# Kernel tuning notes

Measured on AMD Instinct MI355X. Metric: run time of the kernel, lower is better.

## Reference

```python
import jax, jax.numpy as jnp
import numpy as np

HIDDEN = 4096
NH = 32          # query heads
NKV = 2          # kv heads (multi_query_group_num)
HD = 128         # head dim
ROT = HD // 2    # GLM style: rotary applied to first half of head_dim
THETA = 10000.0
SCALE = HD ** -0.5
G = NH // NKV    # query heads per kv group


def _glm_rope(x, positions):
    # x: [B, S, N, HD]; GPT-J interleaved rotation on the first ROT dims.
    inv_freq = 1.0 / (THETA ** (jnp.arange(0, ROT, 2, dtype=jnp.float32) / ROT))  # [ROT//2]
    ang = positions.astype(jnp.float32)[..., None] * inv_freq                      # [B, S, ROT//2]
    cos = jnp.cos(ang)[:, :, None, :]
    sin = jnp.sin(ang)[:, :, None, :]
    xr, xp = x[..., :ROT], x[..., ROT:]
    x1, x2 = xr[..., 0::2], xr[..., 1::2]
    r1 = x1 * cos - x2 * sin
    r2 = x1 * sin + x2 * cos
    xr = jnp.stack([r1, r2], axis=-1).reshape(xr.shape)  # re-interleave
    return jnp.concatenate([xr, xp], axis=-1)


def setup_inputs() -> dict:
    key = jax.random.key(0)
    k1, k2, k3, k4 = jax.random.split(key, 4)
    B, S = 2, 2048
    positions = jnp.broadcast_to(jnp.arange(S, dtype=jnp.int64), (B, S))
    hidden_states = jax.random.normal(k1, (B, S, HIDDEN), dtype=jnp.float32)
    qkv_out = NH * HD + 2 * NKV * HD  # 4608
    w_qkv = jax.random.normal(k2, (qkv_out, HIDDEN), dtype=jnp.float32) * 0.02
    b_qkv = jax.random.normal(k3, (qkv_out,), dtype=jnp.float32) * 0.02
    w_dense = jax.random.normal(k4, (HIDDEN, NH * HD), dtype=jnp.float32) * 0.02
    return {"positions": positions, "hidden_states": hidden_states,
            "w_qkv": w_qkv, "b_qkv": b_qkv, "w_dense": w_dense}


def reference(positions, hidden_states, w_qkv, b_qkv, w_dense):
    B, S, _ = hidden_states.shape
    mixed = hidden_states @ w_qkv.T + b_qkv                      # [B,S,4608]
    q = mixed[..., : NH * HD].reshape(B, S, NH, HD)
    k = mixed[..., NH * HD: NH * HD + NKV * HD].reshape(B, S, NKV, HD)
    v = mixed[..., NH * HD + NKV * HD:].reshape(B, S, NKV, HD)

    q = _glm_rope(q, positions)
    k = _glm_rope(k, positions)

    # GQA: view q as [B, S, NKV, G, HD]
    qg = q.reshape(B, S, NKV, G, HD)
    scores = jnp.einsum('bqkgd,bskd->bkgqs', qg, k) * SCALE      # [B,NKV,G,S,S]
    causal = jnp.tril(jnp.ones((S, S), dtype=bool))
    scores = jnp.where(causal, scores, jnp.finfo(scores.dtype).min)
    probs = jax.nn.softmax(scores, axis=-1)
    ctx = jnp.einsum('bkgqs,bskd->bqkgd', probs, v)              # [B,S,NKV,G,HD]
    ctx = ctx.reshape(B, S, NH * HD)
    return ctx @ w_dense.T                                       # [B,S,HIDDEN]
```

## Files before the change

kernel.cpp:

```cpp
#include <hip/hip_runtime.h>

typedef float f32x4 __attribute__((ext_vector_type(4)));
typedef __bf16 bf16x8 __attribute__((ext_vector_type(8)));
typedef unsigned short u16x4 __attribute__((ext_vector_type(4)));
typedef unsigned short u16x8 __attribute__((ext_vector_type(8)));

#define HIDDEN 4096
#define NH 32
#define NKV 2
#define HD 128
#define SLEN 2048
#define BATCH 2
#define QKV_OUT 4608
#define MROWS 4096
#define ATT_SCALE 0.08838834764831845f
#define KCHUNK 1024

__device__ __forceinline__ unsigned short f2bf(float f) {
  unsigned int u = __float_as_uint(f);
  u += 0x7fffu + ((u >> 16) & 1u);
  return (unsigned short)(u >> 16);
}

__device__ __forceinline__ float bf2f(unsigned short s) {
  return __uint_as_float((unsigned int)s << 16);
}

__device__ __forceinline__ void gload16(const void* g, void* l) {
  __builtin_amdgcn_global_load_lds((const __attribute__((address_space(1))) void*)g,
                                   (__attribute__((address_space(3))) void*)l, 16, 0, 0);
}

__global__ __launch_bounds__(256) void cvt3_f32_bf16(
    const float* __restrict__ s0, unsigned short* __restrict__ d0, int n0,
    const float* __restrict__ s1, unsigned short* __restrict__ d1, int n1,
    const float* __restrict__ s2, unsigned short* __restrict__ d2, int n2) {
  const int ntot = n0 + n1 + n2;
  const int stride = gridDim.x * blockDim.x;
  for (int i = blockIdx.x * blockDim.x + threadIdx.x; i < ntot; i += stride) {
    const float* src;
    unsigned short* dst;
    int j = i;
    if (j < n0) { src = s0; dst = d0; }
    else if (j < n0 + n1) { j -= n0; src = s1; dst = d1; }
    else { j -= n0 + n1; src = s2; dst = d2; }
    float4 v = reinterpret_cast<const float4*>(src)[j];
    u16x4 o;
    o[0] = f2bf(v.x); o[1] = f2bf(v.y); o[2] = f2bf(v.z); o[3] = f2bf(v.w);
    reinterpret_cast<u16x4*>(dst)[j] = o;
  }
}

__global__ __launch_bounds__(512) void gemm_bf16_mfma(
    const unsigned short* __restrict__ A, const unsigned short* __restrict__ B,
    const float* __restrict__ bias, void* __restrict__ Cout, int M, int N, int K,
    int c_bf16) {
  __shared__ unsigned short as_[128 * 32];
  __shared__ unsigned short bs_[256 * 32];
  const int tid = threadIdx.x;
  const int wave = tid >> 6;
  const int lane = tid & 63;
  const int lr = lane & 15, lg = lane >> 4;
  const int m0 = blockIdx.y * 128;
  const int n0 = blockIdx.x * 256;
  const int wm = (wave >> 2) * 64;
  const int wn = (wave & 3) * 64;

  f32x4 acc[4][4] = {};

  const int srow = tid >> 2;
  const int scol = (tid & 3) * 8;
  unsigned short* lA = as_ + wave * 512;
  unsigned short* lB0 = bs_ + wave * 512;
  unsigned short* lB1 = bs_ + 128 * 32 + wave * 512;

  const int nk = K >> 5;
  for (int kt = 0; kt < nk; ++kt) {
    const int kb = kt << 5;
    __syncthreads();
    gload16(A + (size_t)(m0 + srow) * K + kb + scol, lA);
    gload16(B + (size_t)(n0 + srow) * K + kb + scol, lB0);
    gload16(B + (size_t)(n0 + 128 + srow) * K + kb + scol, lB1);
    __syncthreads();

    bf16x8 aF[4], bF[4];
#pragma unroll
    for (int m4 = 0; m4 < 4; ++m4)
      aF[m4] = *reinterpret_cast<const bf16x8*>(
          &as_[(wm + m4 * 16 + lr) * 32 + lg * 8]);
#pragma unroll
    for (int n4 = 0; n4 < 4; ++n4)
      bF[n4] = *reinterpret_cast<const bf16x8*>(
          &bs_[(wn + n4 * 16 + lr) * 32 + lg * 8]);
#pragma unroll
    for (int m4 = 0; m4 < 4; ++m4)
#pragma unroll
      for (int n4 = 0; n4 < 4; ++n4)
        acc[m4][n4] =
            __builtin_amdgcn_mfma_f32_16x16x32_bf16(aF[m4], bF[n4], acc[m4][n4], 0, 0, 0);
  }

#pragma unroll
  for (int m4 = 0; m4 < 4; ++m4) {
#pragma unroll
    for (int n4 = 0; n4 < 4; ++n4) {
      const int col = n0 + wn + n4 * 16 + lr;
      const float bv = bias ? bias[col] : 0.0f;
      if (c_bf16) {
        unsigned short* C = (unsigned short*)Cout;
#pragma unroll
        for (int r = 0; r < 4; ++r) {
          const int row = m0 + wm + m4 * 16 + lg * 4 + r;
          C[(size_t)row * N + col] = f2bf(acc[m4][n4][r] + bv);
        }
      } else {
        float* C = (float*)Cout;
#pragma unroll
        for (int r = 0; r < 4; ++r) {
          const int row = m0 + wm + m4 * 16 + lg * 4 + r;
          C[(size_t)row * N + col] = acc[m4][n4][r] + bv;
        }
      }
    }
  }
}

__global__ __launch_bounds__(256) void prep_qkv(const unsigned short* __restrict__ mixed,
                                                const int* __restrict__ positions,
                                                unsigned short* __restrict__ Qb,
                                                unsigned short* __restrict__ Kb,
                                                unsigned short* __restrict__ Vt) {
  const int m = blockIdx.x;
  const int b = m >> 11, s = m & 2047;
  const float pos = (float)positions[m];
  const int dp = threadIdx.x & 63;
  const bool rope_lane = (dp < 32);
  float sn = 0.0f, cs = 1.0f;
  if (rope_lane) {
    const float inv = __expf(-(float)dp * 0.28782313662425572f);
    sincosf(pos * inv, &sn, &cs);
  }
  const unsigned int* row =
      reinterpret_cast<const unsigned int*>(mixed + (size_t)m * QKV_OUT);
#pragma unroll
  for (int it = 0; it < 9; ++it) {
    const int p = it * 256 + threadIdx.x;
    const int col = p * 2;
    const unsigned int pk = row[p];
    float r1 = bf2f((unsigned short)(pk & 0xffffu));
    float r2 = bf2f((unsigned short)(pk >> 16));
    const int d = col & 127;
    const bool is_v = (col >= NH * HD + NKV * HD);
    if (rope_lane && !is_v) {
      const float x1 = r1, x2 = r2;
      r1 = x1 * cs - x2 * sn;
      r2 = x1 * sn + x2 * cs;
    }
    if (col < NH * HD) {
      r1 *= ATT_SCALE;
      r2 *= ATT_SCALE;
      const int h = col >> 7;
      const unsigned int packed = (unsigned int)f2bf(r1) | ((unsigned int)f2bf(r2) << 16);
      *reinterpret_cast<unsigned int*>(
          &Qb[((size_t)(b * NH + h) * SLEN + s) * HD + d]) = packed;
    } else if (!is_v) {
      const int kv = (col - NH * HD) >> 7;
      const unsigned int packed = (unsigned int)f2bf(r1) | ((unsigned int)f2bf(r2) << 16);
      *reinterpret_cast<unsigned int*>(
          &Kb[((size_t)(b * NKV + kv) * SLEN + s) * HD + d]) = packed;
    } else {
      const int kv = (col - NH * HD - NKV * HD) >> 7;
      unsigned short* vb = Vt + ((size_t)(b * NKV + kv) * HD) * SLEN + s;
      vb[(size_t)d * SLEN] = f2bf(r1);
      vb[(size_t)(d + 1) * SLEN] = f2bf(r2);
    }
  }
}

__global__ __launch_bounds__(512) void flash_mfma(const unsigned short* __restrict__ Qb,
                                                  const unsigned short* __restrict__ Kb,
                                                  const unsigned short* __restrict__ Vt,
                                                  unsigned short* __restrict__ ctx,
                                                  unsigned short* __restrict__ Om,
                                                  float* __restrict__ Ml) {
  __shared__ unsigned short Ks[2][64 * 128];
  __shared__ unsigned short Vs[128 * 64];
  __shared__ unsigned short Ps[8][16 * 64];

  const int tid = threadIdx.x;
  const int wave = tid >> 6, lane = tid & 63;
  const int lr = lane & 15, lg = lane >> 4;

  const int i = blockIdx.x;
  int qt, c;
  if (i < 8) { qt = 15 - i; c = 0; }
  else if (i < 16) { qt = 23 - i; c = 1; }
  else { qt = 23 - i; c = 0; }
  const int h = blockIdx.y, b = blockIdx.z;
  const int kv = h >> 4;
  const int q0 = qt * 128;
  const int s_begin = c * KCHUNK;
  const int s_end = min(KCHUNK * (c + 1), q0 + 128);
  const int nkt = (s_end - s_begin) >> 6;
  const bool single = (c == 0) && (s_end == q0 + 128);
  const int qbw = q0 + wave * 16;

  const unsigned short* Kbase = Kb + (size_t)(b * NKV + kv) * SLEN * HD;
  const unsigned short* Vbase = Vt + (size_t)(b * NKV + kv) * HD * SLEN;

  bf16x8 bQ[4];
  {
    const unsigned short* qp =
        Qb + ((size_t)(b * NH + h) * SLEN + qbw + lr) * HD;
#pragma unroll
    for (int ks = 0; ks < 4; ++ks)
      bQ[ks] = *reinterpret_cast<const bf16x8*>(qp + lg * 8 + ks * 32);
  }

  f32x4 accO[8] = {};
  float mi = -1e30f, li = 0.0f;

  const int vrow_off = lane >> 3, vchunk = lane & 7;
#define STAGE_K(cb, t)                                                                  \
  {                                                                                     \
    const int ss = s_begin + (t) * 64;                                                  \
    _Pragma("unroll") for (int si = 0; si < 2; ++si) {                                  \
      const int krow = wave * 8 + si * 4 + lg;                                          \
      gload16(Kbase + (size_t)(ss + krow) * HD + ((lr ^ (krow & 7)) << 3),              \
              &Ks[cb][(wave * 8 + si * 4) * 128]);                                      \
    }                                                                                   \
  }
#define STAGE_V(t)                                                                      \
  {                                                                                     \
    const int ss = s_begin + (t) * 64;                                                  \
    _Pragma("unroll") for (int si = 0; si < 2; ++si) {                                  \
      const int drow = wave * 16 + si * 8 + vrow_off;                                   \
      gload16(Vbase + (size_t)drow * SLEN + ss + ((vchunk ^ (drow & 7)) << 3),          \
              &Vs[(wave * 16 + si * 8) * 64]);                                          \
    }                                                                                   \
  }

  STAGE_K(0, 0);
  __syncthreads();

  unsigned short* Pw = Ps[wave];

  for (int kt = 0; kt < nkt; ++kt) {
    const int cur = kt & 1;
    const int s0 = s_begin + kt * 64;
    STAGE_V(kt);
    if (kt + 1 < nkt) STAGE_K(cur ^ 1, kt + 1);
    const bool part = (s0 < qbw + 16);

    f32x4 accS[4] = {};
    if (part) {
      bf16x8 aK[4][4];
#pragma unroll
      for (int kb = 0; kb < 4; ++kb)
#pragma unroll
        for (int ks = 0; ks < 4; ++ks)
          aK[kb][ks] = *reinterpret_cast<const bf16x8*>(
              &Ks[cur][(kb * 16 + lr) * 128 + (((ks * 4 + lg) ^ (lr & 7)) << 3)]);
#pragma unroll
      for (int kb = 0; kb < 4; ++kb)
#pragma unroll
        for (int ks = 0; ks < 4; ++ks)
          accS[kb] = __builtin_amdgcn_mfma_f32_16x16x32_bf16(aK[kb][ks], bQ[ks], accS[kb], 0, 0, 0);
    }

    __syncthreads();

    if (part) {
      const int qrow = qbw + lr;
      float v[16];
#pragma unroll
      for (int kb = 0; kb < 4; ++kb)
#pragma unroll
        for (int r = 0; r < 4; ++r) v[kb * 4 + r] = accS[kb][r];
      if (s0 + 63 > qbw) {
#pragma unroll
        for (int kb = 0; kb < 4; ++kb)
#pragma unroll
          for (int r = 0; r < 4; ++r)
            if (s0 + kb * 16 + lg * 4 + r > qrow) v[kb * 4 + r] = -1e30f;
      }
      float m16 = v[0];
#pragma unroll
      for (int i2 = 1; i2 < 16; ++i2) m16 = fmaxf(m16, v[i2]);
      m16 = fmaxf(m16, __shfl_xor(m16, 16));
      m16 = fmaxf(m16, __shfl_xor(m16, 32));
      const float mnew = fmaxf(mi, m16);
      const float cf = __expf(mi - mnew);
      mi = mnew;
      float rs = 0.0f;
#pragma unroll
      for (int i2 = 0; i2 < 16; ++i2) {
        const float p = __expf(v[i2] - mnew);
        v[i2] = p;
        rs += p;
      }
      rs += __shfl_xor(rs, 16);
      rs += __shfl_xor(rs, 32);
      li = li * cf + rs;
#pragma unroll
      for (int n8 = 0; n8 < 8; ++n8) accO[n8] *= cf;
#pragma unroll
      for (int kb = 0; kb < 4; ++kb) {
        const int slot = (kb * 2 + (lg >> 1)) ^ (lr & 7);
        u16x4 pk;
        pk[0] = f2bf(v[kb * 4 + 0]); pk[1] = f2bf(v[kb * 4 + 1]);
        pk[2] = f2bf(v[kb * 4 + 2]); pk[3] = f2bf(v[kb * 4 + 3]);
        *reinterpret_cast<u16x4*>(&Pw[lr * 64 + slot * 8 + (lg & 1) * 4]) = pk;
      }

      bf16x8 pa[2];
#pragma unroll
      for (int ks = 0; ks < 2; ++ks)
        pa[ks] = *reinterpret_cast<const bf16x8*>(
            &Pw[lr * 64 + (((ks * 4 + lg) ^ (lr & 7)) << 3)]);
#pragma unroll
      for (int ks = 0; ks < 2; ++ks) {
#pragma unroll
        for (int n8 = 0; n8 < 8; ++n8) {
          bf16x8 aV = *reinterpret_cast<const bf16x8*>(
              &Vs[(n8 * 16 + lr) * 64 + (((ks * 4 + lg) ^ (lr & 7)) << 3)]);
          accO[n8] = __builtin_amdgcn_mfma_f32_16x16x32_bf16(aV, pa[ks], accO[n8], 0, 0, 0);
        }
      }
    }

    __syncthreads();
  }
#undef STAGE_K
#undef STAGE_V

  if (single) {
    const float inv = 1.0f / li;
    unsigned short* orow =
        ctx + (size_t)(b * SLEN + qbw + lr) * HIDDEN + h * HD + lg * 4;
#pragma unroll
    for (int n8 = 0; n8 < 8; ++n8) {
      u16x4 o;
#pragma unroll
      for (int r = 0; r < 4; ++r) o[r] = f2bf(accO[n8][r] * inv);
      *reinterpret_cast<u16x4*>(orow + n8 * 16) = o;
    }
  } else {
    const int row1k = qbw + lr - 1024;
    const size_t pbase = (size_t)((b * NH + h) * 2 + c) * 1024 + row1k;
    if (lg == 0) {
      Ml[pbase * 2] = mi;
      Ml[pbase * 2 + 1] = li;
    }
    unsigned short* prow = Om + pbase * 128 + lg * 4;
#pragma unroll
    for (int n8 = 0; n8 < 8; ++n8) {
      u16x4 o;
#pragma unroll
      for (int r = 0; r < 4; ++r) o[r] = f2bf(accO[n8][r]);
      *reinterpret_cast<u16x4*>(prow + n8 * 16) = o;
    }
  }
}

__global__ __launch_bounds__(256) void combine_partials(
    const unsigned short* __restrict__ Om, const float* __restrict__ Ml,
    unsigned short* __restrict__ ctx) {
  const int g = blockIdx.x * 64 + (threadIdx.x >> 2);
  const int p = threadIdx.x & 3;
  const int row1k = g & 1023;
  const int h = (g >> 10) & 31;
  const int b = g >> 15;
  const size_t base0 = (size_t)((b * NH + h) * 2 + 0) * 1024 + row1k;
  const size_t base1 = (size_t)((b * NH + h) * 2 + 1) * 1024 + row1k;
  const float m0 = Ml[base0 * 2], l0 = Ml[base0 * 2 + 1];
  const float m1 = Ml[base1 * 2], l1 = Ml[base1 * 2 + 1];
  const float mx = fmaxf(m0, m1);
  const float w0 = __expf(m0 - mx), w1 = __expf(m1 - mx);
  const float inv = 1.0f / (w0 * l0 + w1 * l1);
  const unsigned short* n0 = Om + base0 * 128 + p * 32;
  const unsigned short* n1 = Om + base1 * 128 + p * 32;
  unsigned short* orow =
      ctx + (size_t)(b * SLEN + 1024 + row1k) * HIDDEN + h * HD + p * 32;
#pragma unroll
  for (int cch = 0; cch < 4; ++cch) {
    u16x8 a = *reinterpret_cast<const u16x8*>(n0 + cch * 8);
    u16x8 d = *reinterpret_cast<const u16x8*>(n1 + cch * 8);
    u16x8 o;
#pragma unroll
    for (int j = 0; j < 8; ++j)
      o[j] = f2bf((w0 * bf2f(a[j]) + w1 * bf2f(d[j])) * inv);
    *reinterpret_cast<u16x8*>(orow + cch * 8) = o;
  }
}

extern "C" void kernel_launch(void* const* d_in, const int* in_sizes, int n_in,
                              void* d_out, int out_size, void* d_ws, size_t ws_size,
                              hipStream_t stream) {
  const int* positions = (const int*)d_in[0];
  const float* hidden = (const float*)d_in[1];
  const float* w_qkv = (const float*)d_in[2];
  const float* b_qkv = (const float*)d_in[3];
  const float* w_dense = (const float*)d_in[4];
  float* out = (float*)d_out;

  char* ws = (char*)d_ws;
  size_t off = 0;
  unsigned short* mixed = (unsigned short*)(ws + off);
  off += (size_t)MROWS * QKV_OUT * 4;
  unsigned short* h_bf = (unsigned short*)(ws + off);
  off += (size_t)MROWS * HIDDEN * 2;
  unsigned short* wq_bf = (unsigned short*)(ws + off);
  off += (size_t)QKV_OUT * HIDDEN * 2;
  unsigned short* wd_bf = (unsigned short*)(ws + off);
  off += (size_t)HIDDEN * HIDDEN * 2;
  unsigned short* Kb = (unsigned short*)(ws + off);
  off += (size_t)BATCH * NKV * SLEN * HD * 2;
  unsigned short* Vt = (unsigned short*)(ws + off);
  off += (size_t)BATCH * NKV * SLEN * HD * 2;
  unsigned short* Qb = h_bf;
  unsigned short* ctx_bf = mixed;
  unsigned short* Om = wq_bf;
  float* Ml = (float*)((char*)mixed + 36 * 1024 * 1024);

  cvt3_f32_bf16<<<2048, 256, 0, stream>>>(hidden, h_bf, MROWS * HIDDEN / 4,
                                          w_qkv, wq_bf, QKV_OUT * HIDDEN / 4,
                                          w_dense, wd_bf, HIDDEN * HIDDEN / 4);

  gemm_bf16_mfma<<<dim3(QKV_OUT / 256, MROWS / 128), 512, 0, stream>>>(
      h_bf, wq_bf, b_qkv, mixed, MROWS, QKV_OUT, HIDDEN, 1);

  prep_qkv<<<MROWS, 256, 0, stream>>>(mixed, positions, Qb, Kb, Vt);

  flash_mfma<<<dim3(24, NH, BATCH), 512, 0, stream>>>(Qb, Kb, Vt, ctx_bf, Om, Ml);

  combine_partials<<<1024, 256, 0, stream>>>(Om, Ml, ctx_bf);

  gemm_bf16_mfma<<<dim3(HIDDEN / 256, MROWS / 128), 512, 0, stream>>>(
      ctx_bf, wd_bf, nullptr, out, MROWS, HIDDEN, HIDDEN, 0);
}
```

Baseline: 609.2 us.

## Fuse RoPE/QKV scatter into GEMM epilogue and widen GEMM K-tile with swizzle

```diff
diff --git a/kernel.cpp b/kernel.cpp
--- a/kernel.cpp
+++ b/kernel.cpp
@@ -51,12 +51,23 @@
   }
 }
 
+__global__ __launch_bounds__(256) void build_trig(float2* __restrict__ tab) {
+  const int idx = blockIdx.x * 256 + threadIdx.x;
+  const int p = idx >> 5, j = idx & 31;
+  const float inv = __expf(-(float)j * 0.28782313662425572f);
+  float sn, cs;
+  sincosf((float)p * inv, &sn, &cs);
+  tab[idx] = make_float2(cs, sn);
+}
+
 __global__ __launch_bounds__(512) void gemm_bf16_mfma(
     const unsigned short* __restrict__ A, const unsigned short* __restrict__ B,
     const float* __restrict__ bias, void* __restrict__ Cout, int M, int N, int K,
-    int c_bf16) {
-  __shared__ unsigned short as_[128 * 32];
-  __shared__ unsigned short bs_[256 * 32];
+    int mode, const float2* __restrict__ tab, const int* __restrict__ positions,
+    unsigned short* __restrict__ Qb, unsigned short* __restrict__ Kb,
+    unsigned short* __restrict__ Vt) {
+  __shared__ unsigned short as_[128 * 64];
+  __shared__ unsigned short bs_[256 * 64];
   const int tid = threadIdx.x;
   const int wave = tid >> 6;
   const int lane = tid & 63;
@@ -68,53 +79,52 @@
 
   f32x4 acc[4][4] = {};
 
-  const int srow = tid >> 2;
-  const int scol = (tid & 3) * 8;
+  const int srow8 = tid >> 3;
+  const int schunk = (tid & 7) ^ (srow8 & 7);
+  const int scol = schunk * 8;
   unsigned short* lA = as_ + wave * 512;
-  unsigned short* lB0 = bs_ + wave * 512;
-  unsigned short* lB1 = bs_ + 128 * 32 + wave * 512;
-
-  const int nk = K >> 5;
+  unsigned short* lB = bs_ + wave * 512;
+
+  const int nk = K >> 6;
   for (int kt = 0; kt < nk; ++kt) {
-    const int kb = kt << 5;
+    const int kb = kt << 6;
     __syncthreads();
-    gload16(A + (size_t)(m0 + srow) * K + kb + scol, lA);
-    gload16(B + (size_t)(n0 + srow) * K + kb + scol, lB0);
-    gload16(B + (size_t)(n0 + 128 + srow) * K + kb + scol, lB1);
+    gload16(A + (size_t)(m0 + srow8) * K + kb + scol, lA);
+    gload16(A + (size_t)(m0 + 64 + srow8) * K + kb + scol, lA + 4096);
+    gload16(B + (size_t)(n0 + srow8) * K + kb + scol, lB);
+    gload16(B + (size_t)(n0 + 64 + srow8) * K + kb + scol, lB + 4096);
+    gload16(B + (size_t)(n0 + 128 + srow8) * K + kb + scol, lB + 8192);
+    gload16(B + (size_t)(n0 + 192 + srow8) * K + kb + scol, lB + 12288);
     __syncthreads();
 
-    bf16x8 aF[4], bF[4];
-#pragma unroll
-    for (int m4 = 0; m4 < 4; ++m4)
-      aF[m4] = *reinterpret_cast<const bf16x8*>(
-          &as_[(wm + m4 * 16 + lr) * 32 + lg * 8]);
-#pragma unroll
-    for (int n4 = 0; n4 < 4; ++n4)
-      bF[n4] = *reinterpret_cast<const bf16x8*>(
-          &bs_[(wn + n4 * 16 + lr) * 32 + lg * 8]);
-#pragma unroll
-    for (int m4 = 0; m4 < 4; ++m4)
+#pragma unroll
+    for (int kk = 0; kk < 2; ++kk) {
+      bf16x8 aF[4], bF[4];
+#pragma unroll
+      for (int m4 = 0; m4 < 4; ++m4)
+        aF[m4] = *reinterpret_cast<const bf16x8*>(
+            &as_[(wm + m4 * 16 + lr) * 64 + (((kk * 4 + lg) ^ (lr & 7)) << 3)]);
 #pragma unroll
       for (int n4 = 0; n4 < 4; ++n4)
-        acc[m4][n4] =
-            __builtin_amdgcn_mfma_f32_16x16x32_bf16(aF[m4], bF[n4], acc[m4][n4], 0, 0, 0);
-  }
-
-#pragma unroll
-  for (int m4 = 0; m4 < 4; ++m4) {
-#pragma unroll
-    for (int n4 = 0; n4 < 4; ++n4) {
-      const int col = n0 + wn + n4 * 16 + lr;
-      const float bv = bias ? bias[col] : 0.0f;
-      if (c_bf16) {
-        unsigned short* C = (unsigned short*)Cout;
-#pragma unroll
-        for (int r = 0; r < 4; ++r) {
-          const int row = m0 + wm + m4 * 16 + lg * 4 + r;
-          C[(size_t)row * N + col] = f2bf(acc[m4][n4][r] + bv);
-        }
-      } else {
-        float* C = (float*)Cout;
+        bF[n4] = *reinterpret_cast<const bf16x8*>(
+            &bs_[(wn + n4 * 16 + lr) * 64 + (((kk * 4 + lg) ^ (lr & 7)) << 3)]);
+#pragma unroll
+      for (int m4 = 0; m4 < 4; ++m4)
+#pragma unroll
+        for (int n4 = 0; n4 < 4; ++n4)
+          acc[m4][n4] =
+              __builtin_amdgcn_mfma_f32_16x16x32_bf16(aF[m4], bF[n4], acc[m4][n4], 0, 0, 0);
+    }
+  }
+
+  if (mode == 0) {
+    float* C = (float*)Cout;
+#pragma unroll
+    for (int m4 = 0; m4 < 4; ++m4) {
+#pragma unroll
+      for (int n4 = 0; n4 < 4; ++n4) {
+        const int col = n0 + wn + n4 * 16 + lr;
+        const float bv = bias ? bias[col] : 0.0f;
 #pragma unroll
         for (int r = 0; r < 4; ++r) {
           const int row = m0 + wm + m4 * 16 + lg * 4 + r;
@@ -122,57 +132,54 @@
         }
       }
     }
-  }
-}
-
-__global__ __launch_bounds__(256) void prep_qkv(const unsigned short* __restrict__ mixed,
-                                                const int* __restrict__ positions,
-                                                unsigned short* __restrict__ Qb,
-                                                unsigned short* __restrict__ Kb,
-                                                unsigned short* __restrict__ Vt) {
-  const int m = blockIdx.x;
-  const int b = m >> 11, s = m & 2047;
-  const float pos = (float)positions[m];
-  const int dp = threadIdx.x & 63;
-  const bool rope_lane = (dp < 32);
-  float sn = 0.0f, cs = 1.0f;
-  if (rope_lane) {
-    const float inv = __expf(-(float)dp * 0.28782313662425572f);
-    sincosf(pos * inv, &sn, &cs);
-  }
-  const unsigned int* row =
-      reinterpret_cast<const unsigned int*>(mixed + (size_t)m * QKV_OUT);
-#pragma unroll
-  for (int it = 0; it < 9; ++it) {
-    const int p = it * 256 + threadIdx.x;
-    const int col = p * 2;
-    const unsigned int pk = row[p];
-    float r1 = bf2f((unsigned short)(pk & 0xffffu));
-    float r2 = bf2f((unsigned short)(pk >> 16));
-    const int d = col & 127;
-    const bool is_v = (col >= NH * HD + NKV * HD);
-    if (rope_lane && !is_v) {
-      const float x1 = r1, x2 = r2;
-      r1 = x1 * cs - x2 * sn;
-      r2 = x1 * sn + x2 * cs;
-    }
-    if (col < NH * HD) {
-      r1 *= ATT_SCALE;
-      r2 *= ATT_SCALE;
-      const int h = col >> 7;
-      const unsigned int packed = (unsigned int)f2bf(r1) | ((unsigned int)f2bf(r2) << 16);
-      *reinterpret_cast<unsigned int*>(
-          &Qb[((size_t)(b * NH + h) * SLEN + s) * HD + d]) = packed;
-    } else if (!is_v) {
-      const int kv = (col - NH * HD) >> 7;
-      const unsigned int packed = (unsigned int)f2bf(r1) | ((unsigned int)f2bf(r2) << 16);
-      *reinterpret_cast<unsigned int*>(
-          &Kb[((size_t)(b * NKV + kv) * SLEN + s) * HD + d]) = packed;
-    } else {
-      const int kv = (col - NH * HD - NKV * HD) >> 7;
-      unsigned short* vb = Vt + ((size_t)(b * NKV + kv) * HD) * SLEN + s;
-      vb[(size_t)d * SLEN] = f2bf(r1);
-      vb[(size_t)(d + 1) * SLEN] = f2bf(r2);
+  } else {
+#pragma unroll
+    for (int m4 = 0; m4 < 4; ++m4) {
+      const int rowb = m0 + wm + m4 * 16 + lg * 4;
+      const int bb = rowb >> 11;
+      const int ss = rowb & 2047;
+      int pos[4];
+#pragma unroll
+      for (int r = 0; r < 4; ++r) pos[r] = positions[rowb + r];
+#pragma unroll
+      for (int n4 = 0; n4 < 4; ++n4) {
+        const int col = n0 + wn + n4 * 16 + lr;
+        const float bv = bias[col];
+        float val[4];
+#pragma unroll
+        for (int r = 0; r < 4; ++r) val[r] = acc[m4][n4][r] + bv;
+        const int d = col & 127;
+        const bool isv = (col >= NH * HD + NKV * HD);
+        const bool isq = (col < NH * HD);
+        if (d < 64 && !isv) {
+          const int j = d >> 1;
+#pragma unroll
+          for (int r = 0; r < 4; ++r) {
+            const float2 t = tab[pos[r] * 32 + j];
+            const float other = __shfl_xor(val[r], 1);
+            val[r] = (col & 1) ? (other * t.y + val[r] * t.x)
+                               : (val[r] * t.x - other * t.y);
+          }
+        }
+        if (isq) {
+          const int hh = col >> 7;
+          unsigned short* q = Qb + ((size_t)(bb * NH + hh) * SLEN + ss) * HD + d;
+#pragma unroll
+          for (int r = 0; r < 4; ++r) q[(size_t)r * HD] = f2bf(val[r] * ATT_SCALE);
+        } else if (!isv) {
+          const int kvh = (col - NH * HD) >> 7;
+          unsigned short* k = Kb + ((size_t)(bb * NKV + kvh) * SLEN + ss) * HD + d;
+#pragma unroll
+          for (int r = 0; r < 4; ++r) k[(size_t)r * HD] = f2bf(val[r]);
+        } else {
+          const int kvh = (col - NH * HD - NKV * HD) >> 7;
+          u16x4 o;
+#pragma unroll
+          for (int r = 0; r < 4; ++r) o[r] = f2bf(val[r]);
+          *reinterpret_cast<u16x4*>(
+              &Vt[((size_t)(bb * NKV + kvh) * HD + d) * SLEN + ss]) = o;
+        }
+      }
     }
   }
 }
@@ -210,8 +217,7 @@
 
   bf16x8 bQ[4];
   {
-    const unsigned short* qp =
-        Qb + ((size_t)(b * NH + h) * SLEN + qbw + lr) * HD;
+    const unsigned short* qp = Qb + ((size_t)(b * NH + h) * SLEN + qbw + lr) * HD;
 #pragma unroll
     for (int ks = 0; ks < 4; ++ks)
       bQ[ks] = *reinterpret_cast<const bf16x8*>(qp + lg * 8 + ks * 32);
@@ -418,24 +424,29 @@
   off += (size_t)BATCH * NKV * SLEN * HD * 2;
   unsigned short* Vt = (unsigned short*)(ws + off);
   off += (size_t)BATCH * NKV * SLEN * HD * 2;
+  float2* trig = (float2*)(ws + off);
+  off += (size_t)2048 * 32 * 8;
   unsigned short* Qb = h_bf;
-  unsigned short* ctx_bf = mixed;
+  Qb = mixed;
+  unsigned short* ctx_bf = mixed + (size_t)MROWS * HIDDEN;
   unsigned short* Om = wq_bf;
-  float* Ml = (float*)((char*)mixed + 36 * 1024 * 1024);
+  float* Ml = (float*)(ws + off);
+  off += (size_t)BATCH * NH * 2 * 1024 * 2 * 4;
 
   cvt3_f32_bf16<<<2048, 256, 0, stream>>>(hidden, h_bf, MROWS * HIDDEN / 4,
                                           w_qkv, wq_bf, QKV_OUT * HIDDEN / 4,
                                           w_dense, wd_bf, HIDDEN * HIDDEN / 4);
+  build_trig<<<256, 256, 0, stream>>>(trig);
 
   gemm_bf16_mfma<<<dim3(QKV_OUT / 256, MROWS / 128), 512, 0, stream>>>(
-      h_bf, wq_bf, b_qkv, mixed, MROWS, QKV_OUT, HIDDEN, 1);
-
-  prep_qkv<<<MROWS, 256, 0, stream>>>(mixed, positions, Qb, Kb, Vt);
+      h_bf, wq_bf, b_qkv, nullptr, MROWS, QKV_OUT, HIDDEN, 2, trig, positions,
+      Qb, Kb, Vt);
 
   flash_mfma<<<dim3(24, NH, BATCH), 512, 0, stream>>>(Qb, Kb, Vt, ctx_bf, Om, Ml);
 
   combine_partials<<<1024, 256, 0, stream>>>(Om, Ml, ctx_bf);
 
   gemm_bf16_mfma<<<dim3(HIDDEN / 256, MROWS / 128), 512, 0, stream>>>(
-      ctx_bf, wd_bf, nullptr, out, MROWS, HIDDEN, HIDDEN, 0);
-}
+      ctx_bf, wd_bf, nullptr, out, MROWS, HIDDEN, HIDDEN, 0, nullptr, nullptr,
+      nullptr, nullptr, nullptr);
+}
```

Result: faster. 529.4 us (-13.1%).
